# Performance work log

Hardware: AMD Instinct MI355X
Metric: run time of the kernel (lower is better)

Reference implementation:

```python
import jax, jax.numpy as jnp
import numpy as np

N_NODES = 50000
N_EDGES = 400000
HID = 64
NUM_REL = 230
NUM_TS = 365
SLOPE = 0.2  # LeakyReLU negative slope

def lrelu(v):
    return jnp.where(v >= 0, v, SLOPE * v)

def setup_inputs() -> dict:
    key = jax.random.key(0)
    ks = jax.random.split(key, 10)
    x = jax.random.normal(ks[0], (N_NODES, 2 * HID), dtype=jnp.float32)
    rel_table = jax.random.normal(ks[1], (NUM_REL, HID), dtype=jnp.float32) * 0.1
    time_table = jax.random.normal(ks[2], (NUM_TS, HID), dtype=jnp.float32) * 0.1
    W_rt = jax.random.normal(ks[3], (2 * HID, 2 * HID), dtype=jnp.float32) * (1.0 / np.sqrt(2 * HID))
    b_rt = jnp.zeros((2 * HID,), dtype=jnp.float32)
    W_fc = jax.random.normal(ks[4], (6 * HID, 2 * HID), dtype=jnp.float32) * (1.0 / np.sqrt(6 * HID))
    b_fc = jnp.zeros((2 * HID,), dtype=jnp.float32)
    src = jax.random.randint(ks[5], (N_EDGES,), 0, N_NODES)
    dst = jax.random.randint(ks[6], (N_EDGES,), 0, N_NODES)
    rel = jax.random.randint(ks[7], (N_EDGES,), 0, NUM_REL)
    ts = jax.random.randint(ks[8], (N_EDGES,), 0, NUM_TS)
    edges = jnp.stack([src, dst, rel, ts], axis=1).astype(jnp.int64) if jax.config.jax_enable_x64 else jnp.stack([src, dst, rel, ts], axis=1)
    return {
        "x": x, "rel_table": rel_table, "time_table": time_table,
        "W_rt": W_rt, "b_rt": b_rt, "W_fc": W_fc, "b_fc": b_fc,
        "edges": edges, "num_nodes": N_NODES,
    }

def reference(x, rel_table, time_table, W_rt, b_rt, W_fc, b_fc, edges, num_nodes):
    # MessagePassing.forward + LogicalGNN.aggregated_messages (scatter_mean)
    src, dst, rel, ts = edges[:, 0], edges[:, 1], edges[:, 2], edges[:, 3]
    rel_e = rel_table[rel]          # [E, H]
    time_e = time_table[ts]         # [E, H]
    rel_t = lrelu(jnp.concatenate([rel_e, time_e], axis=-1) @ W_rt + b_rt)  # [E, 2H]
    msg_in = jnp.concatenate([x[src], rel_t, x[dst]], axis=-1)              # [E, 6H]
    messages = lrelu(msg_in @ W_fc + b_fc)                                  # [E, 2H]
    # scatter_mean over dst
    sums = jax.ops.segment_sum(messages, dst, num_segments=num_nodes)       # [N, 2H]
    counts = jax.ops.segment_sum(jnp.ones((messages.shape[0],), messages.dtype), dst, num_segments=num_nodes)
    agg = sums / jnp.maximum(counts, 1.0)[:, None]
    return agg
```

## Files before the change

kernel.cpp:

```cpp
#include <hip/hip_runtime.h>
#include <cstdio>

#define HID 64
#define D 128
#define NUM_REL 230
#define NUM_TS 365
#define NCOMB (NUM_REL*NUM_TS)
#define SLOPE 0.2f
#define XPAD 136
#define MAXDEG 64

typedef __attribute__((ext_vector_type(8))) short short8;
typedef __attribute__((ext_vector_type(4))) float f32x4;

__device__ __forceinline__ float lrelu(float v){ return v >= 0.f ? v : SLOPE*v; }

__device__ __forceinline__ unsigned bf_rne(float f){
    unsigned u = __float_as_uint(f);
    return (u + 0x7fffu + ((u >> 16) & 1u)) >> 16;
}
__device__ __forceinline__ unsigned pk2(float a, float b){
    return bf_rne(a) | (bf_rne(b) << 16);
}
__device__ __forceinline__ float bf_lo(unsigned u){ return __uint_as_float(u << 16); }
__device__ __forceinline__ float bf_hi(unsigned u){ return __uint_as_float(u & 0xffff0000u); }

__global__ __launch_bounds__(256) void k_prep(
        const float* __restrict__ rel_table, const float* __restrict__ time_table,
        const float* __restrict__ W_rt, const float* __restrict__ W_fc,
        const int* __restrict__ edges, int n_edges,
        float* __restrict__ relP, float* __restrict__ timP,
        unsigned short* __restrict__ Wpk13, unsigned short* __restrict__ Wpk2,
        int* __restrict__ deg, int2* __restrict__ ebuf)
{
    int b = blockIdx.x;
    if (b < 298) {
        int row = b*2 + (threadIdx.x >> 7);
        int j   = threadIdx.x & 127;
        if (row >= NUM_REL + NUM_TS) return;
        const float* tbl; const float* Wb; float* out;
        if (row < NUM_REL) { tbl = rel_table + row*HID;            Wb = W_rt;          out = relP + row*D; }
        else               { tbl = time_table + (row-NUM_REL)*HID; Wb = W_rt + HID*D;  out = timP + (row-NUM_REL)*D; }
        float acc = 0.f;
        #pragma unroll
        for (int k = 0; k < HID; ++k) acc += tbl[k] * Wb[k*D + j];
        out[j] = acc;
    } else if (b < 322) {
        int id = (b - 298)*256 + threadIdx.x;
        if (id < 4096) {
            int mt = id >> 8;
            int s  = (id >> 6) & 3;
            int l  = id & 63;
            int m  = mt*16 + (l & 15);
            int kb = s*32 + (l >> 4)*8;
            unsigned short* dst = Wpk13 + ((size_t)(mt*4 + s)*64 + l)*8;
            #pragma unroll
            for (int j = 0; j < 8; ++j) {
                int k = kb + j;
                float v = (m < D) ? W_fc[(size_t)k*D + m]
                                  : W_fc[(size_t)(256 + k)*D + (m - D)];
                dst[j] = (unsigned short)bf_rne(v);
            }
        } else {
            int id2 = id - 4096;
            int mt = id2 >> 8;
            int s  = (id2 >> 6) & 3;
            int l  = id2 & 63;
            int m  = mt*16 + (l & 15);
            int kb = s*32 + (l >> 4)*8;
            unsigned short* dst = Wpk2 + ((size_t)(mt*4 + s)*64 + l)*8;
            #pragma unroll
            for (int j = 0; j < 8; ++j) {
                int k = kb + j;
                dst[j] = (unsigned short)bf_rne(W_fc[(size_t)(D + k)*D + m]);
            }
        }
    } else {
        int e = (b - 322)*256 + threadIdx.x;
        if (e < n_edges) {
            int4 ed = ((const int4*)edges)[e];
            int slot = atomicAdd(&deg[ed.y], 1);
            if (slot < MAXDEG)
                ebuf[(size_t)ed.y*MAXDEG + slot] = make_int2(ed.x, ed.z*NUM_TS + ed.w);
        }
    }
}

__device__ __forceinline__ void xw_body(
        int xb, const float* __restrict__ x,
        const unsigned short* __restrict__ Wpk13,
        unsigned short* __restrict__ xW13bf, int n_nodes,
        unsigned short* Xs )
{
    int t = threadIdx.x;
    int nodeBase = xb*64;
    {
        int row = t >> 2;
        int k0  = (t & 3)*32;
        int node = nodeBase + row;
        unsigned short* dst = Xs + row*XPAD + k0;
        if (node < n_nodes) {
            const float4* src = (const float4*)(x + (size_t)node*D + k0);
            #pragma unroll
            for (int g = 0; g < 8; ++g) {
                float4 v = src[g];
                *(uint2*)(dst + g*4) = make_uint2(pk2(v.x, v.y), pk2(v.z, v.w));
            }
        } else {
            #pragma unroll
            for (int g = 0; g < 8; ++g)
                *(uint2*)(dst + g*4) = make_uint2(0u, 0u);
        }
    }
    __syncthreads();

    int w = t >> 6, l = t & 63;
    int li = l & 15, q = l >> 4;

    f32x4 acc[4][4];
    #pragma unroll
    for (int mi = 0; mi < 4; ++mi)
        #pragma unroll
        for (int ni = 0; ni < 4; ++ni) acc[mi][ni] = (f32x4){0.f,0.f,0.f,0.f};

    #pragma unroll 1
    for (int s = 0; s < 4; ++s) {
        short8 af[4], bf[4];
        #pragma unroll
        for (int mi = 0; mi < 4; ++mi) {
            int mt = w*4 + mi;
            af[mi] = *(const short8*)(Wpk13 + ((size_t)(mt*4 + s)*64 + l)*8);
        }
        #pragma unroll
        for (int ni = 0; ni < 4; ++ni)
            bf[ni] = *(const short8*)(Xs + (ni*16 + li)*XPAD + s*32 + q*8);
        #pragma unroll
        for (int mi = 0; mi < 4; ++mi)
            #pragma unroll
            for (int ni = 0; ni < 4; ++ni)
                acc[mi][ni] = __builtin_amdgcn_mfma_f32_16x16x32_bf16(
                                  af[mi], bf[ni], acc[mi][ni], 0, 0, 0);
    }
    #pragma unroll
    for (int ni = 0; ni < 4; ++ni) {
        int node = nodeBase + ni*16 + li;
        if (node >= n_nodes) continue;
        #pragma unroll
        for (int mi = 0; mi < 4; ++mi) {
            int col = w*64 + mi*16 + q*4;
            *(uint2*)(xW13bf + (size_t)node*256 + col) =
                make_uint2(pk2(acc[mi][ni][0], acc[mi][ni][1]),
                           pk2(acc[mi][ni][2], acc[mi][ni][3]));
        }
    }
}

__device__ __forceinline__ void t2_body(
        int tb, const float* __restrict__ relP, const float* __restrict__ timP,
        const float* __restrict__ b_rt, const unsigned short* __restrict__ Wpk2,
        unsigned short* __restrict__ T2bf,
        unsigned short* Hs )
{
    int t = threadIdx.x;
    int cBase = tb*128;
    {
        int r  = t >> 1;
        int hk = (t & 1)*64;
        int combo = cBase + r;
        if (combo >= NCOMB) combo = NCOMB - 1;
        int rr = combo / NUM_TS;
        int tt = combo - rr*NUM_TS;
        const float4* rv4 = (const float4*)(relP + (size_t)rr*D + hk);
        const float4* tv4 = (const float4*)(timP + (size_t)tt*D + hk);
        const float4* bv4 = (const float4*)(b_rt + hk);
        unsigned short* dst = Hs + r*XPAD + hk;
        #pragma unroll
        for (int g = 0; g < 16; ++g) {
            float4 rv = rv4[g], tv = tv4[g], bv = bv4[g];
            float v0 = lrelu(rv.x+tv.x+bv.x), v1 = lrelu(rv.y+tv.y+bv.y);
            float v2 = lrelu(rv.z+tv.z+bv.z), v3 = lrelu(rv.w+tv.w+bv.w);
            *(uint2*)(dst + g*4) = make_uint2(pk2(v0,v1), pk2(v2,v3));
        }
    }
    __syncthreads();

    int w = t >> 6, l = t & 63;
    int li = l & 15, q = l >> 4;
    int mb = (w & 1)*4;
    int nb = (w >> 1)*64;

    f32x4 acc[4][4];
    #pragma unroll
    for (int mi = 0; mi < 4; ++mi)
        #pragma unroll
        for (int ni = 0; ni < 4; ++ni) acc[mi][ni] = (f32x4){0.f,0.f,0.f,0.f};

    #pragma unroll 1
    for (int s = 0; s < 4; ++s) {
        short8 af[4], bf[4];
        #pragma unroll
        for (int mi = 0; mi < 4; ++mi)
            af[mi] = *(const short8*)(Wpk2 + ((size_t)((mb+mi)*4 + s)*64 + l)*8);
        #pragma unroll
        for (int ni = 0; ni < 4; ++ni)
            bf[ni] = *(const short8*)(Hs + (nb + ni*16 + li)*XPAD + s*32 + q*8);
        #pragma unroll
        for (int mi = 0; mi < 4; ++mi)
            #pragma unroll
            for (int ni = 0; ni < 4; ++ni)
                acc[mi][ni] = __builtin_amdgcn_mfma_f32_16x16x32_bf16(
                                  af[mi], bf[ni], acc[mi][ni], 0, 0, 0);
    }
    #pragma unroll
    for (int ni = 0; ni < 4; ++ni) {
        int combo = cBase + nb + ni*16 + li;
        if (combo >= NCOMB) continue;
        #pragma unroll
        for (int mi = 0; mi < 4; ++mi) {
            int col = (mb + mi)*16 + q*4;
            *(uint2*)(T2bf + (size_t)combo*D + col) =
                make_uint2(pk2(acc[mi][ni][0], acc[mi][ni][1]),
                           pk2(acc[mi][ni][2], acc[mi][ni][3]));
        }
    }
}

__global__ __launch_bounds__(256, 3) void k_mm(
        const float* __restrict__ x, const unsigned short* __restrict__ Wpk13,
        unsigned short* __restrict__ xW13bf, int n_nodes,
        const float* __restrict__ relP, const float* __restrict__ timP,
        const float* __restrict__ b_rt, const unsigned short* __restrict__ Wpk2,
        unsigned short* __restrict__ T2bf, int nxw)
{
    __shared__ __align__(16) unsigned short Hs[128*XPAD];
    int b = blockIdx.x;
    if (b < nxw) {
        xw_body(b, x, Wpk13, xW13bf, n_nodes, Hs);
    } else {
        t2_body(b - nxw, relP, timP, b_rt, Wpk2, T2bf, Hs);
    }
}

__global__ __launch_bounds__(256) void k_agg(
        const int* __restrict__ deg, const int2* __restrict__ ebuf,
        const unsigned short* __restrict__ xW13bf,
        const unsigned short* __restrict__ T2bf,
        const float* __restrict__ b_fc,
        float* __restrict__ out, int n_nodes)
{
    int node = blockIdx.x*4 + (threadIdx.x >> 6);
    int lane = threadIdx.x & 63;
    if (node >= n_nodes) return;
    int dg  = deg[node];
    int cnt = dg < MAXDEG ? dg : MAXDEG;
    const int2* eb = ebuf + (size_t)node*MAXDEG;

    float2 bb = *(const float2*)&b_fc[2*lane];
    unsigned xw3 = *(const unsigned*)&xW13bf[(size_t)node*256 + 128 + 2*lane];
    float base0 = bf_lo(xw3) + bb.x;
    float base1 = bf_hi(xw3) + bb.y;

    float a0 = 0.f, a1 = 0.f, b0 = 0.f, b1 = 0.f;
    float c0 = 0.f, c1 = 0.f, d0 = 0.f, d1 = 0.f;
    int e = 0;
    for (; e + 4 <= cnt; e += 4) {
        int2 e0 = eb[e+0];
        int2 e1 = eb[e+1];
        int2 e2 = eb[e+2];
        int2 e3 = eb[e+3];
        unsigned s0 = *(const unsigned*)&xW13bf[(size_t)e0.x*256 + 2*lane];
        unsigned t0 = *(const unsigned*)&T2bf  [(size_t)e0.y*D   + 2*lane];
        unsigned s1 = *(const unsigned*)&xW13bf[(size_t)e1.x*256 + 2*lane];
        unsigned t1 = *(const unsigned*)&T2bf  [(size_t)e1.y*D   + 2*lane];
        unsigned s2 = *(const unsigned*)&xW13bf[(size_t)e2.x*256 + 2*lane];
        unsigned t2 = *(const unsigned*)&T2bf  [(size_t)e2.y*D   + 2*lane];
        unsigned s3 = *(const unsigned*)&xW13bf[(size_t)e3.x*256 + 2*lane];
        unsigned t3 = *(const unsigned*)&T2bf  [(size_t)e3.y*D   + 2*lane];
        a0 += lrelu(bf_lo(s0) + bf_lo(t0) + base0);
        a1 += lrelu(bf_hi(s0) + bf_hi(t0) + base1);
        b0 += lrelu(bf_lo(s1) + bf_lo(t1) + base0);
        b1 += lrelu(bf_hi(s1) + bf_hi(t1) + base1);
        c0 += lrelu(bf_lo(s2) + bf_lo(t2) + base0);
        c1 += lrelu(bf_hi(s2) + bf_hi(t2) + base1);
        d0 += lrelu(bf_lo(s3) + bf_lo(t3) + base0);
        d1 += lrelu(bf_hi(s3) + bf_hi(t3) + base1);
    }
    for (; e < cnt; ++e) {
        int2 ed = eb[e];
        unsigned u1 = *(const unsigned*)&xW13bf[(size_t)ed.x*256 + 2*lane];
        unsigned u2 = *(const unsigned*)&T2bf  [(size_t)ed.y*D   + 2*lane];
        a0 += lrelu(bf_lo(u1) + bf_lo(u2) + base0);
        a1 += lrelu(bf_hi(u1) + bf_hi(u2) + base1);
    }
    float s0 = (a0 + b0) + (c0 + d0);
    float s1 = (a1 + b1) + (c1 + d1);
    float inv = 1.f / fmaxf((float)dg, 1.f);
    *(float2*)&out[(size_t)node*D + 2*lane] = make_float2(s0*inv, s1*inv);
}

extern "C" void kernel_launch(void* const* d_in, const int* in_sizes, int n_in,
                              void* d_out, int out_size, void* d_ws, size_t ws_size,
                              hipStream_t stream)
{
    const float* x          = (const float*)d_in[0];
    const float* rel_table  = (const float*)d_in[1];
    const float* time_table = (const float*)d_in[2];
    const float* W_rt       = (const float*)d_in[3];
    const float* b_rt       = (const float*)d_in[4];
    const float* W_fc       = (const float*)d_in[5];
    const float* b_fc       = (const float*)d_in[6];
    const int*   edges      = (const int*)d_in[7];

    int n_nodes = in_sizes[0] / D;
    int n_edges = in_sizes[7] / 4;
    int nblkE   = (n_edges + 255) / 256;
    int nxw     = (n_nodes + 63) / 64;
    int nt2     = (NCOMB + 127) / 128;

    char* ws = (char*)d_ws;
    size_t off = 0;
    auto alloc = [&](size_t bytes) -> void* {
        void* p = ws + off; off += (bytes + 255) & ~(size_t)255; return p;
    };
    unsigned short* xW13bf = (unsigned short*)alloc((size_t)n_nodes * 256 * 2);
    unsigned short* T2bf   = (unsigned short*)alloc((size_t)NCOMB * D * 2);
    unsigned short* Wpk13  = (unsigned short*)alloc((size_t)16*4*64*8 * 2);
    unsigned short* Wpk2   = (unsigned short*)alloc((size_t)8*4*64*8 * 2);
    float* relP   = (float*)alloc((size_t)NUM_REL * D * sizeof(float));
    float* timP   = (float*)alloc((size_t)NUM_TS * D * sizeof(float));
    int*   deg    = (int*)alloc((size_t)n_nodes * sizeof(int));
    int2*  ebuf   = (int2*)alloc((size_t)n_nodes * MAXDEG * sizeof(int2));
    if (off > ws_size)
        fprintf(stderr, "kernel_launch: workspace too small: need %zu, have %zu\n", off, ws_size);

    hipMemsetAsync(deg, 0, (size_t)n_nodes * sizeof(int), stream);

    k_prep<<<322 + nblkE, 256, 0, stream>>>(rel_table, time_table, W_rt, W_fc,
                                            edges, n_edges,
                                            relP, timP, Wpk13, Wpk2, deg, ebuf);
    k_mm  <<<nxw + nt2, 256, 0, stream>>>(x, Wpk13, xW13bf, n_nodes,
                                          relP, timP, b_rt, Wpk2, T2bf, nxw);
    k_agg <<<(n_nodes + 3)/4, 256, 0, stream>>>(deg, ebuf, xW13bf, T2bf,
                                                b_fc, (float*)d_out, n_nodes);
}
```

Baseline: 174.2 us.

## Fuse prep, matmul and aggregation into one persistent kernel with grid barriers

```diff
diff --git a/kernel.cpp b/kernel.cpp
--- a/kernel.cpp
+++ b/kernel.cpp
@@ -9,6 +9,7 @@
 #define SLOPE 0.2f
 #define XPAD 136
 #define MAXDEG 64
+#define NBLK 768
 
 typedef __attribute__((ext_vector_type(8))) short short8;
 typedef __attribute__((ext_vector_type(4))) float f32x4;
@@ -25,26 +26,43 @@
 __device__ __forceinline__ float bf_lo(unsigned u){ return __uint_as_float(u << 16); }
 __device__ __forceinline__ float bf_hi(unsigned u){ return __uint_as_float(u & 0xffff0000u); }
 
-__global__ __launch_bounds__(256) void k_prep(
-        const float* __restrict__ rel_table, const float* __restrict__ time_table,
+__device__ __forceinline__ void gbar(int* bar, int gen)
+{
+    __syncthreads();
+    if (threadIdx.x == 0) {
+        __threadfence();
+        int old = atomicAdd(&bar[0], 1);
+        if (old == NBLK*gen - 1) {
+            __hip_atomic_store(&bar[1], gen, __ATOMIC_RELEASE, __HIP_MEMORY_SCOPE_AGENT);
+        } else {
+            while (__hip_atomic_load(&bar[1], __ATOMIC_ACQUIRE, __HIP_MEMORY_SCOPE_AGENT) < gen)
+                __builtin_amdgcn_s_sleep(8);
+        }
+        __threadfence();
+    }
+    __syncthreads();
+}
+
+__device__ __forceinline__ void prep_unit(
+        int b, const float* __restrict__ rel_table, const float* __restrict__ time_table,
         const float* __restrict__ W_rt, const float* __restrict__ W_fc,
         const int* __restrict__ edges, int n_edges,
         float* __restrict__ relP, float* __restrict__ timP,
         unsigned short* __restrict__ Wpk13, unsigned short* __restrict__ Wpk2,
         int* __restrict__ deg, int2* __restrict__ ebuf)
 {
-    int b = blockIdx.x;
     if (b < 298) {
         int row = b*2 + (threadIdx.x >> 7);
         int j   = threadIdx.x & 127;
-        if (row >= NUM_REL + NUM_TS) return;
-        const float* tbl; const float* Wb; float* out;
-        if (row < NUM_REL) { tbl = rel_table + row*HID;            Wb = W_rt;          out = relP + row*D; }
-        else               { tbl = time_table + (row-NUM_REL)*HID; Wb = W_rt + HID*D;  out = timP + (row-NUM_REL)*D; }
-        float acc = 0.f;
-        #pragma unroll
-        for (int k = 0; k < HID; ++k) acc += tbl[k] * Wb[k*D + j];
-        out[j] = acc;
+        if (row < NUM_REL + NUM_TS) {
+            const float* tbl; const float* Wb; float* out;
+            if (row < NUM_REL) { tbl = rel_table + row*HID;            Wb = W_rt;          out = relP + row*D; }
+            else               { tbl = time_table + (row-NUM_REL)*HID; Wb = W_rt + HID*D;  out = timP + (row-NUM_REL)*D; }
+            float acc = 0.f;
+            #pragma unroll
+            for (int k = 0; k < HID; ++k) acc += tbl[k] * Wb[k*D + j];
+            out[j] = acc;
+        }
     } else if (b < 322) {
         int id = (b - 298)*256 + threadIdx.x;
         if (id < 4096) {
@@ -90,7 +108,7 @@
         int xb, const float* __restrict__ x,
         const unsigned short* __restrict__ Wpk13,
         unsigned short* __restrict__ xW13bf, int n_nodes,
-        unsigned short* Xs )
+        unsigned short* Xs)
 {
     int t = threadIdx.x;
     int nodeBase = xb*64;
@@ -153,13 +171,14 @@
                            pk2(acc[mi][ni][2], acc[mi][ni][3]));
         }
     }
+    __syncthreads();
 }
 
 __device__ __forceinline__ void t2_body(
         int tb, const float* __restrict__ relP, const float* __restrict__ timP,
         const float* __restrict__ b_rt, const unsigned short* __restrict__ Wpk2,
         unsigned short* __restrict__ T2bf,
-        unsigned short* Hs )
+        unsigned short* Hs)
 {
     int t = threadIdx.x;
     int cBase = tb*128;
@@ -223,39 +242,22 @@
                            pk2(acc[mi][ni][2], acc[mi][ni][3]));
         }
     }
-}
-
-__global__ __launch_bounds__(256, 3) void k_mm(
-        const float* __restrict__ x, const unsigned short* __restrict__ Wpk13,
-        unsigned short* __restrict__ xW13bf, int n_nodes,
-        const float* __restrict__ relP, const float* __restrict__ timP,
-        const float* __restrict__ b_rt, const unsigned short* __restrict__ Wpk2,
-        unsigned short* __restrict__ T2bf, int nxw)
-{
-    __shared__ __align__(16) unsigned short Hs[128*XPAD];
-    int b = blockIdx.x;
-    if (b < nxw) {
-        xw_body(b, x, Wpk13, xW13bf, n_nodes, Hs);
-    } else {
-        t2_body(b - nxw, relP, timP, b_rt, Wpk2, T2bf, Hs);
-    }
-}
-
-__global__ __launch_bounds__(256) void k_agg(
-        const int* __restrict__ deg, const int2* __restrict__ ebuf,
+    __syncthreads();
+}
+
+__device__ __forceinline__ void agg_unit(
+        int u, const int* __restrict__ deg, const int2* __restrict__ ebuf,
         const unsigned short* __restrict__ xW13bf,
         const unsigned short* __restrict__ T2bf,
-        const float* __restrict__ b_fc,
-        float* __restrict__ out, int n_nodes)
-{
-    int node = blockIdx.x*4 + (threadIdx.x >> 6);
+        float2 bb, float* __restrict__ out, int n_nodes)
+{
+    int node = u*4 + (threadIdx.x >> 6);
     int lane = threadIdx.x & 63;
     if (node >= n_nodes) return;
     int dg  = deg[node];
     int cnt = dg < MAXDEG ? dg : MAXDEG;
     const int2* eb = ebuf + (size_t)node*MAXDEG;
 
-    float2 bb = *(const float2*)&b_fc[2*lane];
     unsigned xw3 = *(const unsigned*)&xW13bf[(size_t)node*256 + 128 + 2*lane];
     float base0 = bf_lo(xw3) + bb.x;
     float base1 = bf_hi(xw3) + bb.y;
@@ -298,6 +300,38 @@
     *(float2*)&out[(size_t)node*D + 2*lane] = make_float2(s0*inv, s1*inv);
 }
 
+__global__ __launch_bounds__(256, 3) void k_fused(
+        const float* __restrict__ x,
+        const float* __restrict__ rel_table, const float* __restrict__ time_table,
+        const float* __restrict__ W_rt, const float* __restrict__ b_rt,
+        const float* __restrict__ W_fc, const float* __restrict__ b_fc,
+        const int* __restrict__ edges, int n_edges, int n_nodes,
+        float* __restrict__ relP, float* __restrict__ timP,
+        unsigned short* __restrict__ Wpk13, unsigned short* __restrict__ Wpk2,
+        unsigned short* __restrict__ xW13bf, unsigned short* __restrict__ T2bf,
+        int* __restrict__ deg, int2* __restrict__ ebuf, int* __restrict__ bar,
+        float* __restrict__ out,
+        int nPrep, int nxw, int nMM, int nAgg)
+{
+    __shared__ __align__(16) unsigned short Hs[128*XPAD];
+
+    for (int u = blockIdx.x; u < nPrep; u += NBLK)
+        prep_unit(u, rel_table, time_table, W_rt, W_fc, edges, n_edges,
+                  relP, timP, Wpk13, Wpk2, deg, ebuf);
+    gbar(bar, 1);
+
+    for (int u = blockIdx.x; u < nMM; u += NBLK) {
+        if (u < nxw) xw_body(u, x, Wpk13, xW13bf, n_nodes, Hs);
+        else         t2_body(u - nxw, relP, timP, b_rt, Wpk2, T2bf, Hs);
+    }
+    gbar(bar, 2);
+
+    int lane = threadIdx.x & 63;
+    float2 bb = *(const float2*)&b_fc[2*lane];
+    for (int u = blockIdx.x; u < nAgg; u += NBLK)
+        agg_unit(u, deg, ebuf, xW13bf, T2bf, bb, out, n_nodes);
+}
+
 extern "C" void kernel_launch(void* const* d_in, const int* in_sizes, int n_in,
                               void* d_out, int out_size, void* d_ws, size_t ws_size,
                               hipStream_t stream)
@@ -316,6 +350,9 @@
     int nblkE   = (n_edges + 255) / 256;
     int nxw     = (n_nodes + 63) / 64;
     int nt2     = (NCOMB + 127) / 128;
+    int nPrep   = 322 + nblkE;
+    int nMM     = nxw + nt2;
+    int nAgg    = (n_nodes + 3) / 4;
 
     char* ws = (char*)d_ws;
     size_t off = 0;
@@ -328,18 +365,18 @@
     unsigned short* Wpk2   = (unsigned short*)alloc((size_t)8*4*64*8 * 2);
     float* relP   = (float*)alloc((size_t)NUM_REL * D * sizeof(float));
     float* timP   = (float*)alloc((size_t)NUM_TS * D * sizeof(float));
-    int*   deg    = (int*)alloc((size_t)n_nodes * sizeof(int));
+    int*   deg    = (int*)alloc((size_t)(n_nodes + 2) * sizeof(int));
     int2*  ebuf   = (int2*)alloc((size_t)n_nodes * MAXDEG * sizeof(int2));
     if (off > ws_size)
         fprintf(stderr, "kernel_launch: workspace too small: need %zu, have %zu\n", off, ws_size);
 
-    hipMemsetAsync(deg, 0, (size_t)n_nodes * sizeof(int), stream);
-
-    k_prep<<<322 + nblkE, 256, 0, stream>>>(rel_table, time_table, W_rt, W_fc,
-                                            edges, n_edges,
-                                            relP, timP, Wpk13, Wpk2, deg, ebuf);
-    k_mm  <<<nxw + nt2, 256, 0, stream>>>(x, Wpk13, xW13bf, n_nodes,
-                                          relP, timP, b_rt, Wpk2, T2bf, nxw);
-    k_agg <<<(n_nodes + 3)/4, 256, 0, stream>>>(deg, ebuf, xW13bf, T2bf,
-                                                b_fc, (float*)d_out, n_nodes);
-}
+    int* bar = deg + n_nodes;
+
+    hipMemsetAsync(deg, 0, (size_t)(n_nodes + 2) * sizeof(int), stream);
+
+    k_fused<<<NBLK, 256, 0, stream>>>(
+        x, rel_table, time_table, W_rt, b_rt, W_fc, b_fc,
+        edges, n_edges, n_nodes,
+        relP, timP, Wpk13, Wpk2, xW13bf, T2bf, deg, ebuf, bar,
+        (float*)d_out, nPrep, nxw, nMM, nAgg);
+}
```

Measured after the change: 594.4 us. 3.41x slower.
